# Kernel optimization log

Hardware: AMD Instinct MI355X
Metric: run time of the kernel (lower is better)

Reference implementation:

```python
import jax, jax.numpy as jnp
jax.config.update("jax_enable_x64", True)
import numpy as np

B, IN_DIM, OUT_DIM = 65536, 256, 256
SCALE = 100.0


def setup_inputs() -> dict:
    key = jax.random.key(0)
    k1, k2, k3 = jax.random.split(key, 3)
    c_x = jax.random.randint(k1, (B, IN_DIM), 0, 200, dtype=jnp.int64)
    weight = jax.random.normal(k2, (OUT_DIM, IN_DIM), dtype=jnp.float32)
    true_bias = jax.random.normal(k3, (OUT_DIM,), dtype=jnp.float32)
    in_scale = jnp.ones((1,), dtype=jnp.float32) * jnp.float32(SCALE)
    return {"c_x": c_x, "weight": weight, "true_bias": true_bias, "in_scale": in_scale}


def scale_round(x, scale):
    # torch.round(x * scale).long()
    return jnp.round(x * scale).astype(jnp.int64)


def reference(c_x, weight, true_bias, in_scale):
    scale = jnp.float32(SCALE)
    s = in_scale[0]
    # quantize weight (done in __init__ in the original) and bias (done per-forward)
    w_q = scale_round(weight, scale)                 # [OUT, IN] int64
    b_q = scale_round(true_bias, s * scale)          # [OUT] int64
    # fhe.matrix_product(W, x.T).T == x @ W.T, then add_matrix_vector adds bias per row
    out = jnp.matmul(c_x, w_q.T) + b_q[None, :]      # [B, OUT] int64
    return out, s * scale
```

## Files before the change

### kernel.cpp

```cpp
#include <hip/hip_runtime.h>

typedef _Float16 half8 __attribute__((ext_vector_type(8)));
typedef _Float16 half4 __attribute__((ext_vector_type(4)));
typedef float floatx4 __attribute__((ext_vector_type(4)));

#define IN_DIM 256
#define OUT_DIM 256
#define M_TILE 32
#define ROWSTR 264

__global__ void quant_kernel(const float* __restrict__ w,
                             const float* __restrict__ bias,
                             const float* __restrict__ in_scale,
                             _Float16* __restrict__ wqp,
                             float* __restrict__ bq,
                             float* __restrict__ out_scalar) {
    int t = blockIdx.x * blockDim.x + threadIdx.x;
    if (t < (OUT_DIM * IN_DIM) / 8) {
        int lane = t & 63;
        int ks   = (t >> 6) & 7;
        int ct   = t >> 9;
        int row  = ct * 16 + (lane & 15);
        int k0   = ks * 32 + (lane >> 4) * 8;
        const float* src = w + row * IN_DIM + k0;
        half8 h;
#pragma unroll
        for (int e = 0; e < 8; ++e)
            h[e] = (_Float16)rintf(src[e] * 100.0f);
        *((half8*)wqp + t) = h;
    }
    if (t < OUT_DIM) {
        float s2 = in_scale[0] * 100.0f;
        bq[t] = rintf(bias[t] * s2);
    }
    if (t == 0 && out_scalar != nullptr)
        out_scalar[0] = in_scale[0] * 100.0f;
}

__global__ __launch_bounds__(256, 4) void gemm_kernel(const int* __restrict__ cx,
                                                      const _Float16* __restrict__ wqp,
                                                      const float* __restrict__ bq,
                                                      float* __restrict__ out) {
    __shared__ _Float16 buf[M_TILE * ROWSTR];

    const int t = threadIdx.x;
    const size_t m0 = (size_t)blockIdx.x * M_TILE;

    const int* cbase = cx + m0 * IN_DIM;
    int4 v[8];
#pragma unroll
    for (int i = 0; i < 8; ++i)
        v[i] = *(const int4*)(cbase + i * 1024 + t * 4);
#pragma unroll
    for (int i = 0; i < 8; ++i) {
        int flat = i * 1024 + t * 4;
        int row = flat >> 8;
        int col = flat & 255;
        half4 h;
        h.x = (_Float16)v[i].x; h.y = (_Float16)v[i].y;
        h.z = (_Float16)v[i].z; h.w = (_Float16)v[i].w;
        *(half4*)&buf[row * ROWSTR + col] = h;
    }
    __syncthreads();

    const int wave = t >> 6;
    const int lane = t & 63;
    const int m16  = lane & 15;
    const int quad = lane >> 4;

    floatx4 acc[4][2] = {};

    const half8* wbase = (const half8*)wqp;
#pragma unroll
    for (int ks = 0; ks < 8; ++ks) {
        half8 afr[4], bfr[2];
#pragma unroll
        for (int i = 0; i < 4; ++i)
            afr[i] = wbase[((wave * 4 + i) * 8 + ks) * 64 + lane];
        const int kb = ks * 32 + quad * 8;
#pragma unroll
        for (int j = 0; j < 2; ++j)
            bfr[j] = *(const half8*)&buf[(j * 16 + m16) * ROWSTR + kb];
#pragma unroll
        for (int i = 0; i < 4; ++i)
#pragma unroll
            for (int j = 0; j < 2; ++j)
                acc[i][j] = __builtin_amdgcn_mfma_f32_16x16x32_f16(afr[i], bfr[j], acc[i][j], 0, 0, 0);
    }

#pragma unroll
    for (int i = 0; i < 4; ++i) {
        int col = wave * 64 + i * 16 + quad * 4;
        floatx4 bv = *(const floatx4*)(bq + col);
#pragma unroll
        for (int j = 0; j < 2; ++j) {
            size_t row = m0 + j * 16 + m16;
            *(floatx4*)(out + row * OUT_DIM + col) = acc[i][j] + bv;
        }
    }
}

extern "C" void kernel_launch(void* const* d_in, const int* in_sizes, int n_in,
                              void* d_out, int out_size, void* d_ws, size_t ws_size,
                              hipStream_t stream) {
    const int*   cx       = (const int*)d_in[0];
    const float* w        = (const float*)d_in[1];
    const float* bias     = (const float*)d_in[2];
    const float* in_scale = (const float*)d_in[3];
    float* out = (float*)d_out;

    _Float16* wqp = (_Float16*)d_ws;
    float*    bq  = (float*)((char*)d_ws + OUT_DIM * IN_DIM * 2);

    const int rows = in_sizes[0] / IN_DIM;
    const size_t gemm_elems = (size_t)rows * OUT_DIM;
    float* out_scalar = ((size_t)out_size > gemm_elems) ? (out + gemm_elems) : nullptr;

    quant_kernel<<<32, 256, 0, stream>>>(w, bias, in_scale, wqp, bq, out_scalar);
    gemm_kernel<<<rows / M_TILE, 256, 0, stream>>>(cx, wqp, bq, out);
}
```

Measured before the change: 131.3 us.

## Load int activation tile directly to LDS with swizzle and convert at fragment read

Stages the int32 input tile with global_load_lds straight into shared memory, using an XOR swizzle of 16-byte chunks to avoid bank conflicts, in place of register staging plus an fp16 store. The int-to-half conversion moves to MFMA fragment reads, and the weight fragments are prefetched one k-step ahead. The goal is to remove the register round-trip and its VGPR pressure. In exchange LDS use doubles to 32KB per block, which may lower occupancy, and the conversion now runs inside the inner loop.

```diff
diff --git a/kernel.cpp b/kernel.cpp
--- a/kernel.cpp
+++ b/kernel.cpp
@@ -1,13 +1,11 @@
 #include <hip/hip_runtime.h>
 
 typedef _Float16 half8 __attribute__((ext_vector_type(8)));
-typedef _Float16 half4 __attribute__((ext_vector_type(4)));
 typedef float floatx4 __attribute__((ext_vector_type(4)));
 
 #define IN_DIM 256
 #define OUT_DIM 256
 #define M_TILE 32
-#define ROWSTR 264
 
 __global__ void quant_kernel(const float* __restrict__ w,
                              const float* __restrict__ bias,
@@ -37,55 +35,79 @@
         out_scalar[0] = in_scale[0] * 100.0f;
 }
 
+__device__ __forceinline__ void gl_lds16(const int* g, int* lds_row_base) {
+    __builtin_amdgcn_global_load_lds(
+        (const __attribute__((address_space(1))) void*)g,
+        (__attribute__((address_space(3))) void*)lds_row_base,
+        16, 0, 0);
+}
+
 __global__ __launch_bounds__(256, 4) void gemm_kernel(const int* __restrict__ cx,
                                                       const _Float16* __restrict__ wqp,
                                                       const float* __restrict__ bq,
                                                       float* __restrict__ out) {
-    __shared__ _Float16 buf[M_TILE * ROWSTR];
+    __shared__ int ctile[M_TILE * IN_DIM];
 
-    const int t = threadIdx.x;
-    const size_t m0 = (size_t)blockIdx.x * M_TILE;
-
-    const int* cbase = cx + m0 * IN_DIM;
-    int4 v[8];
-#pragma unroll
-    for (int i = 0; i < 8; ++i)
-        v[i] = *(const int4*)(cbase + i * 1024 + t * 4);
-#pragma unroll
-    for (int i = 0; i < 8; ++i) {
-        int flat = i * 1024 + t * 4;
-        int row = flat >> 8;
-        int col = flat & 255;
-        half4 h;
-        h.x = (_Float16)v[i].x; h.y = (_Float16)v[i].y;
-        h.z = (_Float16)v[i].z; h.w = (_Float16)v[i].w;
-        *(half4*)&buf[row * ROWSTR + col] = h;
-    }
-    __syncthreads();
-
+    const int t    = threadIdx.x;
     const int wave = t >> 6;
     const int lane = t & 63;
     const int m16  = lane & 15;
     const int quad = lane >> 4;
 
-    floatx4 acc[4][2] = {};
+    const size_t m0 = (size_t)blockIdx.x * M_TILE;
+
+    {
+        const int* gbase = cx + (m0 + wave * 8) * IN_DIM;
+#pragma unroll
+        for (int i = 0; i < 8; ++i) {
+            const int* g = gbase + i * IN_DIM + ((lane ^ i) << 2);
+            gl_lds16(g, &ctile[(wave * 8 + i) * IN_DIM]);
+        }
+    }
 
     const half8* wbase = (const half8*)wqp;
+    half8 acur[4], anext[4];
+#pragma unroll
+    for (int i = 0; i < 4; ++i)
+        acur[i] = wbase[((wave * 4 + i) * 8 + 0) * 64 + lane];
+
+    __syncthreads();
+
+    floatx4 acc[4][2] = {};
+    const int s = m16 & 7;
+
 #pragma unroll
     for (int ks = 0; ks < 8; ++ks) {
-        half8 afr[4], bfr[2];
+        if (ks < 7) {
 #pragma unroll
-        for (int i = 0; i < 4; ++i)
-            afr[i] = wbase[((wave * 4 + i) * 8 + ks) * 64 + lane];
-        const int kb = ks * 32 + quad * 8;
+            for (int i = 0; i < 4; ++i)
+                anext[i] = wbase[((wave * 4 + i) * 8 + (ks + 1)) * 64 + lane];
+        }
+
+        const int pos0 = ((ks * 8 + quad * 2) ^ s) << 2;
+        const int pos1 = pos0 ^ 4;
+        half8 bfr[2];
 #pragma unroll
-        for (int j = 0; j < 2; ++j)
-            bfr[j] = *(const half8*)&buf[(j * 16 + m16) * ROWSTR + kb];
+        for (int j = 0; j < 2; ++j) {
+            const int rb = (j * 16 + m16) * IN_DIM;
+            int4 lo = *(const int4*)&ctile[rb + pos0];
+            int4 hi = *(const int4*)&ctile[rb + pos1];
+            half8 b;
+            b[0] = (_Float16)lo.x; b[1] = (_Float16)lo.y;
+            b[2] = (_Float16)lo.z; b[3] = (_Float16)lo.w;
+            b[4] = (_Float16)hi.x; b[5] = (_Float16)hi.y;
+            b[6] = (_Float16)hi.z; b[7] = (_Float16)hi.w;
+            bfr[j] = b;
+        }
+
 #pragma unroll
         for (int i = 0; i < 4; ++i)
 #pragma unroll
             for (int j = 0; j < 2; ++j)
-                acc[i][j] = __builtin_amdgcn_mfma_f32_16x16x32_f16(afr[i], bfr[j], acc[i][j], 0, 0, 0);
+                acc[i][j] = __builtin_amdgcn_mfma_f32_16x16x32_f16(acur[i], bfr[j], acc[i][j], 0, 0, 0);
+
+#pragma unroll
+        for (int i = 0; i < 4; ++i) acur[i] = anext[i];
     }
 
 #pragma unroll
```

After: 132.5 us. Within noise of the previous version (+0.9%).
